# Kernel optimization log

Hardware: AMD Instinct MI355X
Metric: run time of the kernel (lower is better)

The kernel has to match this reference:

```python
import jax, jax.numpy as jnp
import numpy as np

DIM = 768
HEADS = 12
HEAD_DIM = DIM // HEADS          # 64
DIM_HALF = HEAD_DIM // 2         # 32
SPATIAL = 3


def _rope_cos_sin(grid, voxel_size, theta):
    """grid: static tuple of ints (len SPATIAL); voxel_size: [SPATIAL] float;
    theta: [H, DIM_HALF] per-head frequency spectrum.
    Returns cos, sin of shape [H, N, DIM_HALF] where N = prod(grid)."""
    axes = [jnp.arange(g, dtype=theta.dtype) for g in grid]
    mesh = jnp.meshgrid(*axes, indexing='ij')
    coords = jnp.stack([m.reshape(-1) for m in mesh], axis=-1) * voxel_size  # [N, S] physical coords
    axis_idx = np.arange(DIM_HALF) % len(grid)        # round-robin freq->axis assignment
    pos = coords[:, axis_idx]                          # [N, DIM_HALF]
    ang = pos[None, :, :] * theta[:, None, :]          # [H, N, DIM_HALF]
    return jnp.cos(ang), jnp.sin(ang)


def _rope_apply(t, cos, sin):
    # t: [B, H, N, D]; cos/sin: [H, N, DIM_HALF] broadcast over batch
    t1, t2 = jnp.split(t, 2, axis=-1)
    return jnp.concatenate([t1 * cos - t2 * sin, t1 * sin + t2 * cos], axis=-1)


def setup_inputs() -> dict:
    key = jax.random.key(0)
    k_x, k_qkv, k_proj, k_b = jax.random.split(key, 4)
    B, N = 2, 8 * 16 * 16
    x = jax.random.normal(k_x, (B, N, DIM), dtype=jnp.float32)
    voxel_size = jnp.ones((SPATIAL,), dtype=jnp.float32)
    # nn.Linear weights are [out_features, in_features]
    w_qkv = jax.random.normal(k_qkv, (3 * DIM, DIM), dtype=jnp.float32) * (DIM ** -0.5)
    w_proj = jax.random.normal(k_proj, (DIM, DIM), dtype=jnp.float32) * (DIM ** -0.5)
    b_proj = jax.random.normal(k_b, (DIM,), dtype=jnp.float32) * 0.02
    # learnable per-head base frequencies: theta_j = 10000^{-j/dim_half}
    base = (1.0 / (10000.0 ** (np.arange(DIM_HALF, dtype=np.float32) / DIM_HALF)))
    theta = jnp.asarray(np.tile(base[None, :], (HEADS, 1)))  # [H, DIM_HALF]
    return {"x": x, "voxel_size": voxel_size, "w_qkv": w_qkv, "w_proj": w_proj,
            "b_proj": b_proj, "theta": theta, "grid_d": 8, "grid_h": 16, "grid_w": 16}


def reference(x, voxel_size, w_qkv, w_proj, b_proj, theta, grid_d, grid_h, grid_w):
    B, N, dim = x.shape
    H, D = HEADS, HEAD_DIM
    qkv = jnp.einsum('bnd,ed->bne', x, w_qkv).reshape(B, N, 3, H, D)
    qkv = jnp.transpose(qkv, (2, 0, 3, 1, 4))           # [3, B, H, N, D]
    q, k, v = qkv[0], qkv[1], qkv[2]
    cos, sin = _rope_cos_sin((grid_d, grid_h, grid_w), voxel_size, theta)
    q = _rope_apply(q, cos, sin)
    k = _rope_apply(k, cos, sin)
    scale = 1.0 / np.sqrt(D).astype(np.float32)
    attn = jax.nn.softmax(jnp.einsum('bhnd,bhmd->bhnm', q, k) * scale, axis=-1)
    out = jnp.einsum('bhnm,bhmd->bhnd', attn, v)        # [B, H, N, D]
    out = jnp.transpose(out, (0, 2, 1, 3)).reshape(B, N, dim)
    return out @ w_proj.T + b_proj
```

## Files before the change

### kernel.cpp

```cpp
#include <hip/hip_runtime.h>
#include <stdint.h>

#define DIM 768
#define NHEADS 12
#define HDIM 64
#define DHALF 32
#define NTOK 2048
#define LOG2E 1.44269504088896340736f

typedef unsigned short u16;
typedef unsigned int u32;
typedef __bf16 bf16x8 __attribute__((ext_vector_type(8)));
typedef short s16x8 __attribute__((ext_vector_type(8)));
typedef float f32x4 __attribute__((ext_vector_type(4)));

__device__ __forceinline__ f32x4 f4zero() { f32x4 z = {0.f, 0.f, 0.f, 0.f}; return z; }

__device__ __forceinline__ u16 f2bf(float f) {
    u32 u = __builtin_bit_cast(u32, f);
    u32 r = (u + 0x7FFFu + ((u >> 16) & 1u)) >> 16;
    return (u16)r;
}

__device__ __forceinline__ void gld_lds16(void* lds, const void* g) {
    __builtin_amdgcn_global_load_lds((const __attribute__((address_space(1))) u32*)g,
                                     (__attribute__((address_space(3))) u32*)lds,
                                     16, 0, 0);
}

__global__ __launch_bounds__(256) void cast3_f32_to_bf16(const float* __restrict__ a, u16* __restrict__ oa, int na4,
                                                         const float* __restrict__ b, u16* __restrict__ ob, int nb4,
                                                         const float* __restrict__ c, u16* __restrict__ oc, int nc4) {
    int i = blockIdx.x * 256 + threadIdx.x;
    const float* src;
    u16* dst;
    int j = i;
    if (i < na4) { src = a; dst = oa; }
    else if (i < na4 + nb4) { src = b; dst = ob; j = i - na4; }
    else if (i < na4 + nb4 + nc4) { src = c; dst = oc; j = i - na4 - nb4; }
    else return;
    float4 v = ((const float4*)src)[j];
    u32 w0 = (u32)f2bf(v.x) | ((u32)f2bf(v.y) << 16);
    u32 w1 = (u32)f2bf(v.z) | ((u32)f2bf(v.w) << 16);
    ((uint2*)dst)[j] = make_uint2(w0, w1);
}

__global__ __launch_bounds__(256) void gemm_bt(const u16* __restrict__ A, const u16* __restrict__ Bm,
                                               float* __restrict__ C, const float* __restrict__ bias,
                                               int M, int N, int K) {
    __shared__ __align__(16) u16 sA[128 * 32];
    __shared__ __align__(16) u16 sB[128 * 32];
    const int t = threadIdx.x;
    const int wave = t >> 6, lane = t & 63;
    const int quad = lane >> 4, l16 = lane & 15;
    const int bm = blockIdx.y * 128, bn = blockIdx.x * 128;
    const int wr = wave >> 1, wc = wave & 1;

    f32x4 acc[4][4];
#pragma unroll
    for (int i = 0; i < 4; i++)
#pragma unroll
        for (int j = 0; j < 4; j++) acc[i][j] = f4zero();

    for (int k0 = 0; k0 < K; k0 += 32) {
#pragma unroll
        for (int r = 0; r < 2; ++r) {
            int c = (r * 4 + wave) * 64 + lane;
            int row = c >> 2, kc = c & 3;
            gld_lds16((char*)sA + (size_t)(r * 4 + wave) * 1024,
                      A + (size_t)(bm + row) * K + k0 + kc * 8);
            gld_lds16((char*)sB + (size_t)(r * 4 + wave) * 1024,
                      Bm + (size_t)(bn + row) * K + k0 + kc * 8);
        }
        __syncthreads();
        bf16x8 af[4], bfr[4];
#pragma unroll
        for (int mb = 0; mb < 4; mb++)
            af[mb] = *(const bf16x8*)(sA + (wr * 64 + mb * 16 + l16) * 32 + quad * 8);
#pragma unroll
        for (int nb = 0; nb < 4; nb++)
            bfr[nb] = *(const bf16x8*)(sB + (wc * 64 + nb * 16 + l16) * 32 + quad * 8);
#pragma unroll
        for (int mb = 0; mb < 4; mb++)
#pragma unroll
            for (int nb = 0; nb < 4; nb++)
                acc[mb][nb] = __builtin_amdgcn_mfma_f32_16x16x32_bf16(af[mb], bfr[nb], acc[mb][nb], 0, 0, 0);
        __syncthreads();
    }
#pragma unroll
    for (int mb = 0; mb < 4; mb++)
#pragma unroll
        for (int nb = 0; nb < 4; nb++) {
            int col = bn + wc * 64 + nb * 16 + l16;
            float bv = bias ? bias[col] : 0.f;
#pragma unroll
            for (int r = 0; r < 4; r++) {
                int row = bm + wr * 64 + mb * 16 + quad * 4 + r;
                C[(size_t)row * N + col] = acc[mb][nb][r] + bv;
            }
        }
}

__global__ __launch_bounds__(256) void rope_qk(const float* __restrict__ qkv,
                                               const float* __restrict__ voxel,
                                               const float* __restrict__ theta,
                                               const int* __restrict__ gh_p, const int* __restrict__ gw_p,
                                               u16* __restrict__ q_s, u16* __restrict__ k_s, int B) {
    int tid = blockIdx.x * 256 + threadIdx.x;
    int total = B * NHEADS * NTOK * DHALF;
    if (tid >= total) return;
    int d = tid & (DHALF - 1);
    int n = (tid >> 5) & (NTOK - 1);
    int hb = tid >> 16;
    int h = hb % NHEADS;
    int b = hb / NHEADS;
    int gh = *gh_p, gw = *gw_p;
    int xw = n % gw;
    int rem = n / gw;
    int yh = rem % gh;
    int zd = rem / gh;
    int axis = d % 3;
    float coordv = (axis == 0 ? (float)zd : (axis == 1 ? (float)yh : (float)xw)) * voxel[axis];
    float ang = coordv * theta[h * DHALF + d];
    float s, c;
    __sincosf(ang, &s, &c);
    size_t bi = ((size_t)b * NTOK + n) * (3 * DIM);
    const float* qp = qkv + bi + h * HDIM;
    float q1 = qp[d], q2 = qp[d + DHALF];
    float k1 = qp[DIM + d], k2 = qp[DIM + d + DHALF];
    size_t bh = (size_t)b * NHEADS + h;
    size_t bo = (bh * NTOK + n) * HDIM;
    const float qscale = 0.125f * LOG2E;
    q_s[bo + d] = f2bf((q1 * c - q2 * s) * qscale);
    q_s[bo + d + DHALF] = f2bf((q1 * s + q2 * c) * qscale);
    int tile = n >> 6, r = n & 63, kb = r >> 4, k16 = r & 15;
    size_t kbase = bh * NTOK * HDIM + (size_t)tile * 4096;
    k_s[kbase + (kb * 2 + 0) * 512 + k16 * 32 + d] = f2bf(k1 * c - k2 * s);
    k_s[kbase + (kb * 2 + 1) * 512 + k16 * 32 + d] = f2bf(k1 * s + k2 * c);
}

__global__ __launch_bounds__(256) void v_trans(const float* __restrict__ qkv, u16* __restrict__ vT, int B) {
    __shared__ u16 tile[64][66];
    int nt = blockIdx.x, h = blockIdx.y, b = blockIdx.z;
    int t = threadIdx.x;
    int n_loc = t >> 2, d0 = (t & 3) * 16;
    const float* src = qkv + ((size_t)b * NTOK + nt * 64 + n_loc) * (3 * DIM) + 2 * DIM + h * HDIM + d0;
#pragma unroll
    for (int j = 0; j < 16; j += 4) {
        float4 v = *(const float4*)(src + j);
        tile[n_loc][d0 + j + 0] = f2bf(v.x);
        tile[n_loc][d0 + j + 1] = f2bf(v.y);
        tile[n_loc][d0 + j + 2] = f2bf(v.z);
        tile[n_loc][d0 + j + 3] = f2bf(v.w);
    }
    __syncthreads();
    int dd = t >> 2, q = t & 3;
    size_t bh = (size_t)b * NHEADS + h;
#pragma unroll
    for (int c = 0; c < 2; c++) {
        int kb = c * 32;
        u32 w[4];
        w[0] = (u32)tile[kb + 4 * q + 0][dd] | ((u32)tile[kb + 4 * q + 1][dd] << 16);
        w[1] = (u32)tile[kb + 4 * q + 2][dd] | ((u32)tile[kb + 4 * q + 3][dd] << 16);
        w[2] = (u32)tile[kb + 16 + 4 * q + 0][dd] | ((u32)tile[kb + 16 + 4 * q + 1][dd] << 16);
        w[3] = (u32)tile[kb + 16 + 4 * q + 2][dd] | ((u32)tile[kb + 16 + 4 * q + 3][dd] << 16);
        u16* dst = vT + (((bh * 64 + (size_t)nt * 2 + c) * 64 + dd) * 32) + q * 8;
        *(uint4*)dst = make_uint4(w[0], w[1], w[2], w[3]);
    }
}

__global__ __launch_bounds__(256) void flash_attn(const u16* __restrict__ Q, const u16* __restrict__ Kp,
                                                  const u16* __restrict__ Vp, u16* __restrict__ Out) {
    int i = blockIdx.x;
    int bh_i = i % 24;
    int qt = i / 24;
    int b = bh_i / NHEADS, h = bh_i % NHEADS;
    int t = threadIdx.x, wave = t >> 6, lane = t & 63, quad = lane >> 4, l16 = lane & 15;
    size_t bh = (size_t)b * NHEADS + h;
    const u16* Qb = Q + bh * NTOK * HDIM;
    const u16* Kb = Kp + bh * NTOK * HDIM;
    const u16* Vb = Vp + bh * NTOK * HDIM;

    __shared__ __align__(16) u16 sK[4096];
    __shared__ __align__(16) u16 sV[4096];

    const int q0 = qt * 128 + wave * 32;
    bf16x8 qf[2][2];
#pragma unroll
    for (int qb = 0; qb < 2; qb++)
#pragma unroll
        for (int kc = 0; kc < 2; kc++)
            qf[qb][kc] = *(const bf16x8*)(Qb + (size_t)(q0 + qb * 16 + l16) * HDIM + kc * 32 + quad * 8);

    s16x8 ov;
#pragma unroll
    for (int j = 0; j < 8; j++) ov[j] = (l16 == 0) ? (short)0x3F80 : (short)0;

    f32x4 o[2][5];
#pragma unroll
    for (int qb = 0; qb < 2; qb++)
#pragma unroll
        for (int db = 0; db < 5; db++) o[qb][db] = f4zero();

    for (int kt = 0; kt < NTOK / 64; ++kt) {
        const u16* Kg = Kb + (size_t)kt * 4096;
        const u16* Vg = Vb + (size_t)kt * 4096;
        gld_lds16((char*)sK + wave * 1024, Kg + wave * 512 + lane * 8);
        gld_lds16((char*)sK + 4096 + wave * 1024, Kg + 2048 + wave * 512 + lane * 8);
        gld_lds16((char*)sV + wave * 1024, Vg + wave * 512 + lane * 8);
        gld_lds16((char*)sV + 4096 + wave * 1024, Vg + 2048 + wave * 512 + lane * 8);
        __syncthreads();
#pragma unroll
        for (int c = 0; c < 2; ++c) {
            bf16x8 kf[2][2];
#pragma unroll
            for (int kb2 = 0; kb2 < 2; kb2++)
#pragma unroll
                for (int kc = 0; kc < 2; kc++)
                    kf[kb2][kc] = *(const bf16x8*)(sK + ((c * 2 + kb2) * 2 + kc) * 512 + l16 * 32 + quad * 8);
            s16x8 bv[4];
#pragma unroll
            for (int db = 0; db < 4; db++)
                bv[db] = *(const s16x8*)(sV + c * 2048 + (db * 16 + l16) * 32 + quad * 8);
            f32x4 st[2][2];
#pragma unroll
            for (int qb = 0; qb < 2; qb++)
#pragma unroll
                for (int kb2 = 0; kb2 < 2; kb2++) {
                    f32x4 z = f4zero();
                    z = __builtin_amdgcn_mfma_f32_16x16x32_bf16(kf[kb2][0], qf[qb][0], z, 0, 0, 0);
                    st[qb][kb2] = __builtin_amdgcn_mfma_f32_16x16x32_bf16(kf[kb2][1], qf[qb][1], z, 0, 0, 0);
                }
#pragma unroll
            for (int qb = 0; qb < 2; qb++) {
                bf16x8 pb;
#pragma unroll
                for (int r = 0; r < 4; r++) {
                    pb[r] = (__bf16)__builtin_exp2f(st[qb][0][r]);
                    pb[r + 4] = (__bf16)__builtin_exp2f(st[qb][1][r]);
                }
#pragma unroll
                for (int db = 0; db < 4; db++)
                    o[qb][db] = __builtin_amdgcn_mfma_f32_16x16x32_bf16(pb, __builtin_bit_cast(bf16x8, bv[db]),
                                                                        o[qb][db], 0, 0, 0);
                o[qb][4] = __builtin_amdgcn_mfma_f32_16x16x32_bf16(pb, __builtin_bit_cast(bf16x8, ov),
                                                                   o[qb][4], 0, 0, 0);
            }
        }
        __syncthreads();
    }

#pragma unroll
    for (int qb = 0; qb < 2; qb++)
#pragma unroll
        for (int r = 0; r < 4; r++) {
            float s = __shfl(o[qb][4][r], lane & 48);
            float inv = 1.0f / s;
            int n = q0 + qb * 16 + quad * 4 + r;
            u16* dst = Out + ((size_t)b * NTOK + n) * DIM + h * HDIM + l16;
#pragma unroll
            for (int db = 0; db < 4; db++)
                dst[db * 16] = f2bf(o[qb][db][r] * inv);
        }
}

extern "C" void kernel_launch(void* const* d_in, const int* in_sizes, int n_in,
                              void* d_out, int out_size, void* d_ws, size_t ws_size,
                              hipStream_t stream) {
    const float* x = (const float*)d_in[0];
    const float* voxel = (const float*)d_in[1];
    const float* w_qkv = (const float*)d_in[2];
    const float* w_proj = (const float*)d_in[3];
    const float* b_proj = (const float*)d_in[4];
    const float* theta = (const float*)d_in[5];
    const int* gh_p = (const int*)d_in[7];
    const int* gw_p = (const int*)d_in[8];
    const int B = in_sizes[0] / (NTOK * DIM);
    const int M = B * NTOK;

    char* p = (char*)d_ws;
    u16* xb = (u16*)p;       p += (size_t)M * DIM * 2;
    u16* wqkvb = (u16*)p;    p += (size_t)3 * DIM * DIM * 2;
    u16* wprojb = (u16*)p;   p += (size_t)DIM * DIM * 2;
    float* qkv = (float*)p;  p += (size_t)M * 3 * DIM * 4;
    u16* q_s = (u16*)p;      p += (size_t)M * DIM * 2;
    u16* k_s = (u16*)p;      p += (size_t)M * DIM * 2;
    u16* vT = (u16*)p;       p += (size_t)M * DIM * 2;
    u16* attn = (u16*)p;     p += (size_t)M * DIM * 2;

    int na4 = M * DIM / 4, nb4 = 3 * DIM * DIM / 4, nc4 = DIM * DIM / 4;
    cast3_f32_to_bf16<<<dim3((na4 + nb4 + nc4 + 255) / 256), 256, 0, stream>>>(
        x, xb, na4, w_qkv, wqkvb, nb4, w_proj, wprojb, nc4);

    gemm_bt<<<dim3(3 * DIM / 128, M / 128), 256, 0, stream>>>(xb, wqkvb, qkv, nullptr, M, 3 * DIM, DIM);

    int total = B * NHEADS * NTOK * DHALF;
    rope_qk<<<dim3((total + 255) / 256), 256, 0, stream>>>(qkv, voxel, theta, gh_p, gw_p, q_s, k_s, B);
    v_trans<<<dim3(NTOK / 64, NHEADS, B), 256, 0, stream>>>(qkv, vT, B);
    flash_attn<<<dim3((B * NHEADS * NTOK) / 128), 256, 0, stream>>>(q_s, k_s, vT, attn);
    gemm_bt<<<dim3(DIM / 128, M / 128), 256, 0, stream>>>(attn, wprojb, (float*)d_out, b_proj, M, DIM, DIM);
}
```

Baseline: 213.5 us.

## Double-buffer flash attention K/V tiles, widen query tile, fuse rope and V prep

Flash attention now prefetches the next K/V tile into a second LDS buffer while the current one is computed. Each wave handles 64 queries instead of 32, so each block covers 256 queries. K and V are stored in a lane-contiguous layout so fragment loads are linear per lane. The rope and V-transpose kernels are merged into one launch. The larger query tile halves the grid to 192 blocks and adds register pressure (launch_bounds 256,1), which may leave part of the GPU idle.

```diff
diff --git a/kernel.cpp b/kernel.cpp
--- a/kernel.cpp
+++ b/kernel.cpp
@@ -101,79 +101,87 @@
         }
 }
 
-__global__ __launch_bounds__(256) void rope_qk(const float* __restrict__ qkv,
-                                               const float* __restrict__ voxel,
-                                               const float* __restrict__ theta,
-                                               const int* __restrict__ gh_p, const int* __restrict__ gw_p,
-                                               u16* __restrict__ q_s, u16* __restrict__ k_s, int B) {
-    int tid = blockIdx.x * 256 + threadIdx.x;
-    int total = B * NHEADS * NTOK * DHALF;
-    if (tid >= total) return;
-    int d = tid & (DHALF - 1);
-    int n = (tid >> 5) & (NTOK - 1);
-    int hb = tid >> 16;
-    int h = hb % NHEADS;
-    int b = hb / NHEADS;
-    int gh = *gh_p, gw = *gw_p;
-    int xw = n % gw;
-    int rem = n / gw;
-    int yh = rem % gh;
-    int zd = rem / gh;
-    int axis = d % 3;
-    float coordv = (axis == 0 ? (float)zd : (axis == 1 ? (float)yh : (float)xw)) * voxel[axis];
-    float ang = coordv * theta[h * DHALF + d];
-    float s, c;
-    __sincosf(ang, &s, &c);
-    size_t bi = ((size_t)b * NTOK + n) * (3 * DIM);
-    const float* qp = qkv + bi + h * HDIM;
-    float q1 = qp[d], q2 = qp[d + DHALF];
-    float k1 = qp[DIM + d], k2 = qp[DIM + d + DHALF];
-    size_t bh = (size_t)b * NHEADS + h;
-    size_t bo = (bh * NTOK + n) * HDIM;
-    const float qscale = 0.125f * LOG2E;
-    q_s[bo + d] = f2bf((q1 * c - q2 * s) * qscale);
-    q_s[bo + d + DHALF] = f2bf((q1 * s + q2 * c) * qscale);
-    int tile = n >> 6, r = n & 63, kb = r >> 4, k16 = r & 15;
-    size_t kbase = bh * NTOK * HDIM + (size_t)tile * 4096;
-    k_s[kbase + (kb * 2 + 0) * 512 + k16 * 32 + d] = f2bf(k1 * c - k2 * s);
-    k_s[kbase + (kb * 2 + 1) * 512 + k16 * 32 + d] = f2bf(k1 * s + k2 * c);
-}
-
-__global__ __launch_bounds__(256) void v_trans(const float* __restrict__ qkv, u16* __restrict__ vT, int B) {
+__global__ __launch_bounds__(256) void prep(const float* __restrict__ qkv,
+                                            const float* __restrict__ voxel,
+                                            const float* __restrict__ theta,
+                                            const int* __restrict__ gh_p, const int* __restrict__ gw_p,
+                                            u16* __restrict__ q_s, u16* __restrict__ k_s,
+                                            u16* __restrict__ vT, int B, int nrope) {
     __shared__ u16 tile[64][66];
-    int nt = blockIdx.x, h = blockIdx.y, b = blockIdx.z;
+    int bid = blockIdx.x;
     int t = threadIdx.x;
-    int n_loc = t >> 2, d0 = (t & 3) * 16;
-    const float* src = qkv + ((size_t)b * NTOK + nt * 64 + n_loc) * (3 * DIM) + 2 * DIM + h * HDIM + d0;
-#pragma unroll
-    for (int j = 0; j < 16; j += 4) {
-        float4 v = *(const float4*)(src + j);
-        tile[n_loc][d0 + j + 0] = f2bf(v.x);
-        tile[n_loc][d0 + j + 1] = f2bf(v.y);
-        tile[n_loc][d0 + j + 2] = f2bf(v.z);
-        tile[n_loc][d0 + j + 3] = f2bf(v.w);
+    if (bid < nrope) {
+        int tid = bid * 256 + t;
+        int d = tid & (DHALF - 1);
+        int n = (tid >> 5) & (NTOK - 1);
+        int hb = tid >> 16;
+        int h = hb % NHEADS;
+        int b = hb / NHEADS;
+        int gh = *gh_p, gw = *gw_p;
+        int xw = n % gw;
+        int rem = n / gw;
+        int yh = rem % gh;
+        int zd = rem / gh;
+        int axis = d % 3;
+        float coordv = (axis == 0 ? (float)zd : (axis == 1 ? (float)yh : (float)xw)) * voxel[axis];
+        float ang = coordv * theta[h * DHALF + d];
+        float s, c;
+        __sincosf(ang, &s, &c);
+        size_t bi = ((size_t)b * NTOK + n) * (3 * DIM);
+        const float* qp = qkv + bi + h * HDIM;
+        float q1 = qp[d], q2 = qp[d + DHALF];
+        float k1 = qp[DIM + d], k2 = qp[DIM + d + DHALF];
+        size_t bh = (size_t)b * NHEADS + h;
+        size_t bo = (bh * NTOK + n) * HDIM;
+        const float qscale = 0.125f * LOG2E;
+        q_s[bo + d] = f2bf((q1 * c - q2 * s) * qscale);
+        q_s[bo + d + DHALF] = f2bf((q1 * s + q2 * c) * qscale);
+        int tile_i = n >> 6, r = n & 63, g = r >> 4, k16 = r & 15;
+        int qd = d >> 3, j = d & 7;
+        size_t off = bh * NTOK * HDIM + (size_t)tile_i * 4096 +
+                     (size_t)(g * 2) * 512 + (qd * 16 + k16) * 8 + j;
+        k_s[off] = f2bf(k1 * c - k2 * s);
+        k_s[off + 512] = f2bf(k1 * s + k2 * c);
+    } else {
+        int idx = bid - nrope;
+        int nt = idx & 31;
+        int rem = idx >> 5;
+        int h = rem % NHEADS, b = rem / NHEADS;
+        int n_loc = t >> 2, d0 = (t & 3) * 16;
+        const float* src = qkv + ((size_t)b * NTOK + nt * 64 + n_loc) * (3 * DIM) + 2 * DIM + h * HDIM + d0;
+#pragma unroll
+        for (int j = 0; j < 16; j += 4) {
+            float4 v = *(const float4*)(src + j);
+            tile[n_loc][d0 + j + 0] = f2bf(v.x);
+            tile[n_loc][d0 + j + 1] = f2bf(v.y);
+            tile[n_loc][d0 + j + 2] = f2bf(v.z);
+            tile[n_loc][d0 + j + 3] = f2bf(v.w);
+        }
+        __syncthreads();
+        int db = t >> 6, l = t & 63, q = (t >> 4) & 3, l16 = t & 15;
+        int dd = db * 16 + l16;
+        size_t bh = (size_t)b * NHEADS + h;
+#pragma unroll
+        for (int c = 0; c < 2; c++) {
+            u32 w[4];
+#pragma unroll
+            for (int jp = 0; jp < 4; jp++) {
+                int jj0 = jp * 2, jj1 = jp * 2 + 1;
+                int key0 = c * 32 + (jj0 < 4 ? 4 * q + jj0 : 16 + 4 * q + jj0 - 4);
+                int key1 = c * 32 + (jj1 < 4 ? 4 * q + jj1 : 16 + 4 * q + jj1 - 4);
+                w[jp] = (u32)tile[key0][dd] | ((u32)tile[key1][dd] << 16);
+            }
+            u16* dst = vT + ((bh * 64 + (size_t)nt * 2 + c) * 2048 + db * 512 + (size_t)l * 8);
+            *(uint4*)dst = make_uint4(w[0], w[1], w[2], w[3]);
+        }
     }
-    __syncthreads();
-    int dd = t >> 2, q = t & 3;
-    size_t bh = (size_t)b * NHEADS + h;
-#pragma unroll
-    for (int c = 0; c < 2; c++) {
-        int kb = c * 32;
-        u32 w[4];
-        w[0] = (u32)tile[kb + 4 * q + 0][dd] | ((u32)tile[kb + 4 * q + 1][dd] << 16);
-        w[1] = (u32)tile[kb + 4 * q + 2][dd] | ((u32)tile[kb + 4 * q + 3][dd] << 16);
-        w[2] = (u32)tile[kb + 16 + 4 * q + 0][dd] | ((u32)tile[kb + 16 + 4 * q + 1][dd] << 16);
-        w[3] = (u32)tile[kb + 16 + 4 * q + 2][dd] | ((u32)tile[kb + 16 + 4 * q + 3][dd] << 16);
-        u16* dst = vT + (((bh * 64 + (size_t)nt * 2 + c) * 64 + dd) * 32) + q * 8;
-        *(uint4*)dst = make_uint4(w[0], w[1], w[2], w[3]);
-    }
-}
-
-__global__ __launch_bounds__(256) void flash_attn(const u16* __restrict__ Q, const u16* __restrict__ Kp,
-                                                  const u16* __restrict__ Vp, u16* __restrict__ Out) {
+}
+
+__global__ __launch_bounds__(256, 1) void flash_attn(const u16* __restrict__ Q, const u16* __restrict__ Kp,
+                                                     const u16* __restrict__ Vp, u16* __restrict__ Out, int NBH) {
     int i = blockIdx.x;
-    int bh_i = i % 24;
-    int qt = i / 24;
+    int bh_i = i % NBH;
+    int qt = i / NBH;
     int b = bh_i / NHEADS, h = bh_i % NHEADS;
     int t = threadIdx.x, wave = t >> 6, lane = t & 63, quad = lane >> 4, l16 = lane & 15;
     size_t bh = (size_t)b * NHEADS + h;
@@ -181,13 +189,12 @@
     const u16* Kb = Kp + bh * NTOK * HDIM;
     const u16* Vb = Vp + bh * NTOK * HDIM;
 
-    __shared__ __align__(16) u16 sK[4096];
-    __shared__ __align__(16) u16 sV[4096];
-
-    const int q0 = qt * 128 + wave * 32;
-    bf16x8 qf[2][2];
-#pragma unroll
-    for (int qb = 0; qb < 2; qb++)
+    __shared__ __align__(16) u16 smem[2][8192];
+
+    const int q0 = qt * 256 + wave * 64;
+    bf16x8 qf[4][2];
+#pragma unroll
+    for (int qb = 0; qb < 4; qb++)
 #pragma unroll
         for (int kc = 0; kc < 2; kc++)
             qf[qb][kc] = *(const bf16x8*)(Qb + (size_t)(q0 + qb * 16 + l16) * HDIM + kc * 32 + quad * 8);
@@ -196,20 +203,29 @@
 #pragma unroll
     for (int j = 0; j < 8; j++) ov[j] = (l16 == 0) ? (short)0x3F80 : (short)0;
 
-    f32x4 o[2][5];
-#pragma unroll
-    for (int qb = 0; qb < 2; qb++)
+    f32x4 o[4][5];
+#pragma unroll
+    for (int qb = 0; qb < 4; qb++)
 #pragma unroll
         for (int db = 0; db < 5; db++) o[qb][db] = f4zero();
 
-    for (int kt = 0; kt < NTOK / 64; ++kt) {
+    auto stage = [&](int kt, int bi) {
         const u16* Kg = Kb + (size_t)kt * 4096;
         const u16* Vg = Vb + (size_t)kt * 4096;
-        gld_lds16((char*)sK + wave * 1024, Kg + wave * 512 + lane * 8);
-        gld_lds16((char*)sK + 4096 + wave * 1024, Kg + 2048 + wave * 512 + lane * 8);
-        gld_lds16((char*)sV + wave * 1024, Vg + wave * 512 + lane * 8);
-        gld_lds16((char*)sV + 4096 + wave * 1024, Vg + 2048 + wave * 512 + lane * 8);
+        u16* buf = &smem[bi][0];
+        gld_lds16(buf + (2 * wave + 0) * 512, Kg + (2 * wave + 0) * 512 + lane * 8);
+        gld_lds16(buf + (2 * wave + 1) * 512, Kg + (2 * wave + 1) * 512 + lane * 8);
+        gld_lds16(buf + 4096 + (2 * wave + 0) * 512, Vg + (2 * wave + 0) * 512 + lane * 8);
+        gld_lds16(buf + 4096 + (2 * wave + 1) * 512, Vg + (2 * wave + 1) * 512 + lane * 8);
+    };
+
+    stage(0, 0);
+    int cur = 0;
+    for (int kt = 0; kt < NTOK / 64; ++kt) {
         __syncthreads();
+        if (kt + 1 < NTOK / 64) stage(kt + 1, cur ^ 1);
+        const u16* sK = &smem[cur][0];
+        const u16* sV = &smem[cur][4096];
 #pragma unroll
         for (int c = 0; c < 2; ++c) {
             bf16x8 kf[2][2];
@@ -217,41 +233,41 @@
             for (int kb2 = 0; kb2 < 2; kb2++)
 #pragma unroll
                 for (int kc = 0; kc < 2; kc++)
-                    kf[kb2][kc] = *(const bf16x8*)(sK + ((c * 2 + kb2) * 2 + kc) * 512 + l16 * 32 + quad * 8);
+                    kf[kb2][kc] = *(const bf16x8*)(sK + ((c * 2 + kb2) * 2 + kc) * 512 + lane * 8);
             s16x8 bv[4];
 #pragma unroll
             for (int db = 0; db < 4; db++)
-                bv[db] = *(const s16x8*)(sV + c * 2048 + (db * 16 + l16) * 32 + quad * 8);
-            f32x4 st[2][2];
-#pragma unroll
-            for (int qb = 0; qb < 2; qb++)
-#pragma unroll
-                for (int kb2 = 0; kb2 < 2; kb2++) {
+                bv[db] = *(const s16x8*)(sV + c * 2048 + db * 512 + lane * 8);
+#pragma unroll
+            for (int qb = 0; qb < 4; qb++) {
+                f32x4 st0, st1;
+                {
                     f32x4 z = f4zero();
-                    z = __builtin_amdgcn_mfma_f32_16x16x32_bf16(kf[kb2][0], qf[qb][0], z, 0, 0, 0);
-                    st[qb][kb2] = __builtin_amdgcn_mfma_f32_16x16x32_bf16(kf[kb2][1], qf[qb][1], z, 0, 0, 0);
+                    z = __builtin_amdgcn_mfma_f32_16x16x32_bf16(kf[0][0], qf[qb][0], z, 0, 0, 0);
+                    st0 = __builtin_amdgcn_mfma_f32_16x16x32_bf16(kf[0][1], qf[qb][1], z, 0, 0, 0);
+                    f32x4 z2 = f4zero();
+                    z2 = __builtin_amdgcn_mfma_f32_16x16x32_bf16(kf[1][0], qf[qb][0], z2, 0, 0, 0);
+                    st1 = __builtin_amdgcn_mfma_f32_16x16x32_bf16(kf[1][1], qf[qb][1], z2, 0, 0, 0);
                 }
-#pragma unroll
-            for (int qb = 0; qb < 2; qb++) {
                 bf16x8 pb;
 #pragma unroll
                 for (int r = 0; r < 4; r++) {
-                    pb[r] = (__bf16)__builtin_exp2f(st[qb][0][r]);
-                    pb[r + 4] = (__bf16)__builtin_exp2f(st[qb][1][r]);
+                    pb[r] = (__bf16)__builtin_exp2f(st0[r]);
+                    pb[r + 4] = (__bf16)__builtin_exp2f(st1[r]);
                 }
 #pragma unroll
                 for (int db = 0; db < 4; db++)
                     o[qb][db] = __builtin_amdgcn_mfma_f32_16x16x32_bf16(pb, __builtin_bit_cast(bf16x8, bv[db]),
-                                                                        o[qb][db], 0, 0, 0);
+                                                                       o[qb][db], 0, 0, 0);
                 o[qb][4] = __builtin_amdgcn_mfma_f32_16x16x32_bf16(pb, __builtin_bit_cast(bf16x8, ov),
-                                                                   o[qb][4], 0, 0, 0);
+                                                                  o[qb][4], 0, 0, 0);
             }
         }
-        __syncthreads();
+        cur ^= 1;
     }
 
 #pragma unroll
-    for (int qb = 0; qb < 2; qb++)
+    for (int qb = 0; qb < 4; qb++)
 #pragma unroll
         for (int r = 0; r < 4; r++) {
             float s = __shfl(o[qb][4][r], lane & 48);
@@ -294,9 +310,11 @@
 
     gemm_bt<<<dim3(3 * DIM / 128, M / 128), 256, 0, stream>>>(xb, wqkvb, qkv, nullptr, M, 3 * DIM, DIM);
 
-    int total = B * NHEADS * NTOK * DHALF;
-    rope_qk<<<dim3((total + 255) / 256), 256, 0, stream>>>(qkv, voxel, theta, gh_p, gw_p, q_s, k_s, B);
-    v_trans<<<dim3(NTOK / 64, NHEADS, B), 256, 0, stream>>>(qkv, vT, B);
-    flash_attn<<<dim3((B * NHEADS * NTOK) / 128), 256, 0, stream>>>(q_s, k_s, vT, attn);
+    int nrope = (B * NHEADS * NTOK * DHALF) / 256;
+    int nvt = B * NHEADS * (NTOK / 64);
+    prep<<<dim3(nrope + nvt), 256, 0, stream>>>(qkv, voxel, theta, gh_p, gw_p, q_s, k_s, vT, B, nrope);
+
+    flash_attn<<<dim3((B * NHEADS * NTOK) / 256), 256, 0, stream>>>(q_s, k_s, vT, attn, B * NHEADS);
+
     gemm_bt<<<dim3(DIM / 128, M / 128), 256, 0, stream>>>(attn, wprojb, (float*)d_out, b_proj, M, DIM, DIM);
 }
```

Result: slower. 223.2 us (+4.6%).
